# Kernel optimization log

Measured on AMD Instinct MI355X. Metric: run time of the kernel, lower is better.

The kernel has to match this reference:

```python
import jax, jax.numpy as jnp
import numpy as np

B, S, DM = 8, 1024, 1024
H, DH = 16, 64  # num_heads, per-head dim (q=k=v=r)
SCALE = 64 ** 1 / 2  # faithful to source: d_k**1/2 == d_k/2 == 32.0


def setup_inputs() -> dict:
    key = jax.random.key(0)
    ks = jax.random.split(key, 13)
    std = 1.0 / np.sqrt(DM)
    def lin(k):
        kw, kb = jax.random.split(k)
        W = jax.random.uniform(kw, (DM, H * DH), jnp.float32, -std, std)
        b = jax.random.uniform(kb, (H * DH,), jnp.float32, -std, std)
        return W, b
    Wq, bq = lin(ks[0]); Wk, bk = lin(ks[1]); Wv, bv = lin(ks[2]); Wr, br = lin(ks[3])
    Wo = jax.random.uniform(ks[4], (H * DH, DM), jnp.float32, -std, std)
    bo = jax.random.uniform(ks[5], (DM,), jnp.float32, -std, std)
    return {
        "value": jax.random.normal(ks[6], (B, S, DM), jnp.float32),
        "key": jax.random.normal(ks[7], (B, S, DM), jnp.float32),
        "query": jax.random.normal(ks[8], (B, S, DM), jnp.float32),
        "Wq": Wq, "bq": bq, "Wk": Wk, "bk": bk,
        "Wv": Wv, "bv": bv, "Wr": Wr, "br": br,
        "Wo": Wo, "bo": bo,
    }


def reference(value, key, query, Wq, bq, Wk, bk, Wv, bv, Wr, br, Wo, bo):
    b = query.shape[0]
    # projections -> [b, s, h, d] -> [b, h, s, d]
    q = (query @ Wq + bq).reshape(b, -1, H, DH).transpose(0, 2, 1, 3)
    k = (key @ Wk + bk).reshape(b, -1, H, DH).transpose(0, 2, 1, 3)
    v = (value @ Wv + bv).reshape(b, -1, H, DH).transpose(0, 2, 1, 3)
    r = (query @ Wr + br).reshape(b, -1, H, DH).transpose(0, 2, 1, 3)
    energy = jnp.einsum('bhid,bhjd->bhij', q, k)
    attn = jax.nn.softmax(energy / SCALE, axis=-1)
    ctx = jnp.einsum('bhjd,bhij->bhid', v, attn)
    gated = (ctx * r).transpose(0, 2, 1, 3)  # R-gating, back to [b, s, h, d]
    out = gated.reshape(b, -1, H * DH) @ Wo + bo
    return out
```

## Files before the change

kernel.cpp:

```cpp
#include <hip/hip_runtime.h>
#include <stdint.h>

#define B_ 8
#define S_ 1024
#define DM_ 1024
#define H_ 16
#define DH_ 64
#define M_ (B_*S_)

typedef unsigned short u16;
typedef unsigned int u32;
typedef __attribute__((ext_vector_type(8))) short bf16x8;
typedef __attribute__((ext_vector_type(4))) float f32x4;

__device__ __forceinline__ u16 f2bf(float f){
  union { float f; u32 u; } x; x.f = f;
  u32 r = x.u + 0x7fffu + ((x.u >> 16) & 1u);
  return (u16)(r >> 16);
}
__device__ __forceinline__ float bf2f(u16 u){
  union { u32 u; float f; } x; x.u = ((u32)u) << 16; return x.f;
}
__device__ __forceinline__ u32 cvtpk(float lo, float hi){
  u32 r; asm("v_cvt_pk_bf16_f32 %0, %1, %2" : "=v"(r) : "v"(lo), "v"(hi)); return r;
}
__device__ __forceinline__ void gload16(const void* g, void* l){
  __builtin_amdgcn_global_load_lds((const __attribute__((address_space(1))) void*)g,
                                   (__attribute__((address_space(3))) void*)l, 16, 0, 0);
}

__global__ void k_cvt_act(const float* __restrict__ v, const float* __restrict__ k,
                          const float* __restrict__ q, u16* __restrict__ vb,
                          u16* __restrict__ kb, u16* __restrict__ qb){
  int z = blockIdx.y;
  const float* src = (z == 0) ? v : (z == 1) ? k : q;
  u16* dst = (z == 0) ? vb : (z == 1) ? kb : qb;
  size_t i = ((size_t)blockIdx.x * blockDim.x + threadIdx.x) * 8;
  float4 a = *(const float4*)(src + i);
  float4 b = *(const float4*)(src + i + 4);
  uint4 o;
  o.x = (u32)f2bf(a.x) | ((u32)f2bf(a.y) << 16);
  o.y = (u32)f2bf(a.z) | ((u32)f2bf(a.w) << 16);
  o.z = (u32)f2bf(b.x) | ((u32)f2bf(b.y) << 16);
  o.w = (u32)f2bf(b.z) | ((u32)f2bf(b.w) << 16);
  *(uint4*)(dst + i) = o;
}

__global__ void k_cvt_wt(const float* __restrict__ w0, const float* __restrict__ w1,
                         const float* __restrict__ w2, const float* __restrict__ w3,
                         const float* __restrict__ w4,
                         u16* __restrict__ wall, u16* __restrict__ wot){
  __shared__ float tile[32][33];
  int z = blockIdx.z;
  const float* src = (z==0)?w0:(z==1)?w1:(z==2)?w2:(z==3)?w3:w4;
  u16* dst = (z<4) ? (wall + (size_t)z * 1048576) : wot;
  int n0 = blockIdx.x * 32, k0 = blockIdx.y * 32;
  int tx = threadIdx.x, ty = threadIdx.y;
#pragma unroll
  for (int i=0;i<4;i++) tile[ty+8*i][tx] = src[(size_t)(k0+ty+8*i)*DM_ + n0+tx];
  __syncthreads();
#pragma unroll
  for (int i=0;i<4;i++) dst[(size_t)(n0+ty+8*i)*DM_ + k0+tx] = f2bf(tile[tx][ty+8*i]);
}

__global__ __launch_bounds__(256) void k_proj(const u16* __restrict__ qb, const u16* __restrict__ kb,
                                              const u16* __restrict__ vb, const u16* __restrict__ wall,
                                              const float* __restrict__ bqp, const float* __restrict__ brp,
                                              const float* __restrict__ bkp, const float* __restrict__ bvp,
                                              u16* __restrict__ qpj, u16* __restrict__ rpj,
                                              u16* __restrict__ kpj, u16* __restrict__ vtg){
  __shared__ u16 As[128*64];
  __shared__ u16 Bs[128*64];
  const int tid = threadIdx.x;
  const int w = tid >> 6, l = tid & 63, g = l >> 4, s = l & 15;
  const int wr = w >> 1, wc = w & 1;
  const int m0 = blockIdx.x << 7;
  const int ng0 = blockIdx.y << 7;
  const int chunk = ng0 >> 10;
  const u16* A = (chunk < 2) ? qb : (chunk == 2) ? kb : vb;
  const float* bias = (chunk==0)?bqp:(chunk==1)?brp:(chunk==2)?bkp:bvp;
  f32x4 acc[4][4];
#pragma unroll
  for (int i=0;i<4;i++)
#pragma unroll
    for (int j=0;j<4;j++) acc[i][j] = (f32x4){0.f,0.f,0.f,0.f};

  for (int k0 = 0; k0 < 1024; k0 += 64){
    __syncthreads();
#pragma unroll
    for (int i=0;i<4;i++){
      int c = tid + i*256;
      int m = c >> 3, slot = c & 7;
      gload16(A + ((size_t)(m0+m) << 10) + (k0 + ((slot ^ (m & 7)) << 3)),
              &As[(i*256 + w*64) * 8]);
    }
#pragma unroll
    for (int i=0;i<4;i++){
      int c = tid + i*256;
      int n = c >> 3, slot = c & 7;
      gload16(wall + ((size_t)(ng0+n) << 10) + (k0 + ((slot ^ (n & 7)) << 3)),
              &Bs[(i*256 + w*64) * 8]);
    }
    __syncthreads();
#pragma unroll
    for (int ks=0; ks<2; ks++){
      bf16x8 af[4], bfv[4];
#pragma unroll
      for (int mi=0;mi<4;mi++){
        int m = wr*64 + mi*16 + s;
        af[mi] = *(const bf16x8*)&As[m*64 + (((ks*4+g) ^ (s & 7)) << 3)];
      }
#pragma unroll
      for (int ni=0;ni<4;ni++){
        int n = wc*64 + ni*16 + s;
        bfv[ni] = *(const bf16x8*)&Bs[n*64 + (((ks*4+g) ^ (s & 7)) << 3)];
      }
#pragma unroll
      for (int mi=0;mi<4;mi++)
#pragma unroll
        for (int ni=0;ni<4;ni++)
          acc[mi][ni] = __builtin_amdgcn_mfma_f32_16x16x32_bf16(af[mi], bfv[ni], acc[mi][ni], 0, 0, 0);
    }
  }
  u16* outp = (chunk==0)?qpj:(chunk==1)?rpj:kpj;
#pragma unroll
  for (int ni=0;ni<4;ni++){
    int cg = ng0 + wc*64 + ni*16 + s;
    int col = cg & 1023;
    float bv = bias[col];
#pragma unroll
    for (int mi=0;mi<4;mi++){
      int row = m0 + wr*64 + mi*16 + g*4;
      if (chunk == 3){
        union { short4 v; u16 e[4]; } pk;
#pragma unroll
        for (int r=0;r<4;r++) pk.e[r] = f2bf(acc[mi][ni][r] + bv);
        size_t vrow = ((size_t)(row >> 10) * 16 + (col >> 6)) * 64 + (col & 63);
        *(short4*)&vtg[(vrow << 10) + (row & 1023)] = pk.v;
      } else {
#pragma unroll
        for (int r=0;r<4;r++)
          outp[((size_t)(row+r) << 10) + col] = f2bf(acc[mi][ni][r] + bv);
      }
    }
  }
}

__global__ __launch_bounds__(256) void k_gemm_out(const u16* __restrict__ A, const u16* __restrict__ Bt,
                                                  const float* __restrict__ bias, float* __restrict__ Out){
  __shared__ u16 As[128*64];
  __shared__ u16 Bs[128*64];
  const int tid = threadIdx.x;
  const int w = tid >> 6, l = tid & 63, g = l >> 4, s = l & 15;
  const int wr = w >> 1, wc = w & 1;
  const int m0 = blockIdx.x << 7, n0 = blockIdx.y << 7;
  f32x4 acc[4][4];
#pragma unroll
  for (int i=0;i<4;i++)
#pragma unroll
    for (int j=0;j<4;j++) acc[i][j] = (f32x4){0.f,0.f,0.f,0.f};

  for (int k0 = 0; k0 < 1024; k0 += 64){
    __syncthreads();
#pragma unroll
    for (int i=0;i<4;i++){
      int c = tid + i*256;
      int m = c >> 3, slot = c & 7;
      gload16(A + ((size_t)(m0+m) << 10) + (k0 + ((slot ^ (m & 7)) << 3)),
              &As[(i*256 + w*64) * 8]);
    }
#pragma unroll
    for (int i=0;i<4;i++){
      int c = tid + i*256;
      int n = c >> 3, slot = c & 7;
      gload16(Bt + ((size_t)(n0+n) << 10) + (k0 + ((slot ^ (n & 7)) << 3)),
              &Bs[(i*256 + w*64) * 8]);
    }
    __syncthreads();
#pragma unroll
    for (int ks=0; ks<2; ks++){
      bf16x8 af[4], bfv[4];
#pragma unroll
      for (int mi=0;mi<4;mi++){
        int m = wr*64 + mi*16 + s;
        af[mi] = *(const bf16x8*)&As[m*64 + (((ks*4+g) ^ (s & 7)) << 3)];
      }
#pragma unroll
      for (int ni=0;ni<4;ni++){
        int n = wc*64 + ni*16 + s;
        bfv[ni] = *(const bf16x8*)&Bs[n*64 + (((ks*4+g) ^ (s & 7)) << 3)];
      }
#pragma unroll
      for (int mi=0;mi<4;mi++)
#pragma unroll
        for (int ni=0;ni<4;ni++)
          acc[mi][ni] = __builtin_amdgcn_mfma_f32_16x16x32_bf16(af[mi], bfv[ni], acc[mi][ni], 0, 0, 0);
    }
  }
#pragma unroll
  for (int ni=0;ni<4;ni++){
    int col = n0 + wc*64 + ni*16 + s;
    float bv = bias[col];
#pragma unroll
    for (int mi=0;mi<4;mi++){
      int row = m0 + wr*64 + mi*16 + g*4;
#pragma unroll
      for (int r=0;r<4;r++)
        Out[((size_t)(row+r) << 10) + col] = acc[mi][ni][r] + bv;
    }
  }
}

__global__ __launch_bounds__(256) void k_attn(const u16* __restrict__ qp, const u16* __restrict__ kp,
                                              const u16* __restrict__ vtg, const u16* __restrict__ rp,
                                              u16* __restrict__ gated){
  __shared__ u16 Ks[2][64*64];
  __shared__ u16 Vs[2][64*64];
  __shared__ u32 PsU[4*16*32];
  const int tid = threadIdx.x;
  const int w = tid >> 6, l = tid & 63, g = l >> 4, s = l & 15;
  const int bid = blockIdx.x;
  const int swz = (bid & 7) * 256 + (bid >> 3);
  const int q0 = (swz & 15) << 6;
  const int bh = swz >> 4;
  const int b = bh >> 4, h = bh & 15;
  const size_t base = ((size_t)b << 20);
  const int colh = h << 6;
  const float KL = 1.4426950408889634f / 32.0f;

  const size_t qoff = base + ((size_t)(q0 + w*16 + s) << 10) + colh;
  bf16x8 qf0 = *(const bf16x8*)(qp + qoff + g*8);
  bf16x8 qf1 = *(const bf16x8*)(qp + qoff + 32 + g*8);
  const size_t vbase = ((size_t)(b*16 + h)) << 16;

  u32* PsW = PsU + (w << 9);
  const int sx2 = s << 1;

  float mrun = -1e30f, lsum = 0.f;
  f32x4 of[4];
#pragma unroll
  for (int d=0;d<4;d++) of[d] = (f32x4){0.f,0.f,0.f,0.f};

#define STAGE_KV(BUF, KV0) do { \
    _Pragma("unroll") \
    for (int i=0;i<2;i++){ \
      int c = tid + i*256; \
      int sj = c >> 3, slot = c & 7; \
      gload16(kp + base + ((size_t)((KV0)+sj) << 10) + colh + ((slot ^ (sj & 7)) << 3), \
              &Ks[BUF][(i*256 + w*64) * 8]); \
    } \
    _Pragma("unroll") \
    for (int i=0;i<2;i++){ \
      int c = tid + i*256; \
      int d = c >> 3, slot = c & 7; \
      gload16(vtg + vbase + ((size_t)d << 10) + (KV0) + ((slot ^ (d & 7)) << 3), \
              &Vs[BUF][(i*256 + w*64) * 8]); \
    } \
  } while(0)

  STAGE_KV(0, 0);
  __syncthreads();

  int cur = 0;
  for (int t = 0; t < 16; t++){
    if (t < 15) STAGE_KV(cur ^ 1, (t+1) << 6);
    const u16* ksb = Ks[cur];
    const u16* vsb = Vs[cur];

    f32x4 e2[4];
#pragma unroll
    for (int sjf=0;sjf<4;sjf++){
      e2[sjf] = (f32x4){0.f,0.f,0.f,0.f};
      int sj = sjf*16 + s;
      bf16x8 kf0 = *(const bf16x8*)&ksb[sj*64 + ((g ^ (s & 7)) << 3)];
      e2[sjf] = __builtin_amdgcn_mfma_f32_16x16x32_bf16(kf0, qf0, e2[sjf], 0, 0, 0);
      bf16x8 kf1 = *(const bf16x8*)&ksb[sj*64 + (((4+g) ^ (s & 7)) << 3)];
      e2[sjf] = __builtin_amdgcn_mfma_f32_16x16x32_bf16(kf1, qf1, e2[sjf], 0, 0, 0);
    }
    float rm = fmaxf(fmaxf(e2[0][0], e2[0][1]), e2[0][2]);
    rm = fmaxf(fmaxf(rm, e2[0][3]), e2[1][0]);
    rm = fmaxf(fmaxf(rm, e2[1][1]), e2[1][2]);
    rm = fmaxf(fmaxf(rm, e2[1][3]), e2[2][0]);
    rm = fmaxf(fmaxf(rm, e2[2][1]), e2[2][2]);
    rm = fmaxf(fmaxf(rm, e2[2][3]), e2[3][0]);
    rm = fmaxf(fmaxf(rm, e2[3][1]), e2[3][2]);
    rm = fmaxf(rm, e2[3][3]);
    rm = fmaxf(rm, __shfl_xor(rm, 16, 64));
    rm = fmaxf(rm, __shfl_xor(rm, 32, 64));
    if (!__all(rm <= mrun + 177.0f)){
      float nm = fmaxf(mrun, rm);
      float alpha = __builtin_amdgcn_exp2f((mrun - nm) * KL);
      mrun = nm;
      lsum *= alpha;
      float ac[4];
#pragma unroll
      for (int r=0;r<4;r++) ac[r] = __shfl(alpha, g*4 + r, 64);
#pragma unroll
      for (int d=0; d<4; d++)
#pragma unroll
        for (int r=0;r<4;r++) of[d][r] *= ac[r];
    }

    const float mk = mrun * KL;
#pragma unroll
    for (int sjf=0;sjf<4;sjf++){
      float p0 = __builtin_amdgcn_exp2f(e2[sjf][0]*KL - mk);
      float p1 = __builtin_amdgcn_exp2f(e2[sjf][1]*KL - mk);
      float p2 = __builtin_amdgcn_exp2f(e2[sjf][2]*KL - mk);
      float p3 = __builtin_amdgcn_exp2f(e2[sjf][3]*KL - mk);
      lsum += (p0 + p1) + (p2 + p3);
      uint2 pk; pk.x = cvtpk(p0, p1); pk.y = cvtpk(p2, p3);
      int phys = (8*sjf + 2*g) ^ sx2;
      *reinterpret_cast<uint2*>(&PsW[(s << 5) + phys]) = pk;
    }
    union { u32 u[4]; bf16x8 v; } pa0, pa1;
    {
      uint2 r0 = *reinterpret_cast<const uint2*>(&PsW[(s << 5) + ((4*g    ) ^ sx2)]);
      uint2 r1 = *reinterpret_cast<const uint2*>(&PsW[(s << 5) + ((4*g + 2) ^ sx2)]);
      pa0.u[0] = r0.x; pa0.u[1] = r0.y; pa0.u[2] = r1.x; pa0.u[3] = r1.y;
      uint2 r2 = *reinterpret_cast<const uint2*>(&PsW[(s << 5) + ((16 + 4*g    ) ^ sx2)]);
      uint2 r3 = *reinterpret_cast<const uint2*>(&PsW[(s << 5) + ((16 + 4*g + 2) ^ sx2)]);
      pa1.u[0] = r2.x; pa1.u[1] = r2.y; pa1.u[2] = r3.x; pa1.u[3] = r3.y;
    }
#pragma unroll
    for (int df=0; df<4; df++){
      int d = df*16 + s;
      bf16x8 v0 = *(const bf16x8*)&vsb[d*64 + ((g ^ (s & 7)) << 3)];
      bf16x8 v1 = *(const bf16x8*)&vsb[d*64 + (((4+g) ^ (s & 7)) << 3)];
      of[df] = __builtin_amdgcn_mfma_f32_16x16x32_bf16(pa0.v, v0, of[df], 0, 0, 0);
      of[df] = __builtin_amdgcn_mfma_f32_16x16x32_bf16(pa1.v, v1, of[df], 0, 0, 0);
    }
    __syncthreads();
    cur ^= 1;
  }
#undef STAGE_KV

  lsum += __shfl_xor(lsum, 16, 64);
  lsum += __shfl_xor(lsum, 32, 64);
  float inv = 1.0f / lsum;
  float ic[4];
#pragma unroll
  for (int r=0;r<4;r++) ic[r] = __shfl(inv, g*4 + r, 64);
#pragma unroll
  for (int df=0; df<4; df++){
#pragma unroll
    for (int r=0;r<4;r++){
      size_t row = (size_t)(q0 + w*16 + g*4 + r);
      size_t idx = base + (row << 10) + colh + df*16 + s;
      float o = of[df][r] * ic[r];
      float rg = bf2f(rp[idx]);
      gated[idx] = f2bf(o * rg);
    }
  }
}

extern "C" void kernel_launch(void* const* d_in, const int* in_sizes, int n_in,
                              void* d_out, int out_size, void* d_ws, size_t ws_size,
                              hipStream_t stream){
  (void)in_sizes; (void)n_in; (void)out_size; (void)ws_size;
  const float* value = (const float*)d_in[0];
  const float* key   = (const float*)d_in[1];
  const float* query = (const float*)d_in[2];
  const float* Wq = (const float*)d_in[3];  const float* bq = (const float*)d_in[4];
  const float* Wk = (const float*)d_in[5];  const float* bk = (const float*)d_in[6];
  const float* Wv = (const float*)d_in[7];  const float* bv = (const float*)d_in[8];
  const float* Wr = (const float*)d_in[9];  const float* br = (const float*)d_in[10];
  const float* Wo = (const float*)d_in[11]; const float* bo = (const float*)d_in[12];

  char* ws = (char*)d_ws;
  const size_t MB = (size_t)1 << 20;
  u16* qb   = (u16*)(ws + 0*MB);
  u16* kb   = (u16*)(ws + 16*MB);
  u16* vb   = (u16*)(ws + 32*MB);
  u16* wall = (u16*)(ws + 48*MB);
  u16* wot  = (u16*)(ws + 56*MB);
  u16* qpj  = (u16*)(ws + 58*MB);
  u16* kpj  = (u16*)(ws + 74*MB);
  u16* vtg  = (u16*)(ws + 90*MB);
  u16* rpj  = (u16*)(ws + 106*MB);
  u16* gat  = qb;

  k_cvt_act<<<dim3(4096, 3), 256, 0, stream>>>(value, key, query, vb, kb, qb);
  k_cvt_wt<<<dim3(32, 32, 5), dim3(32, 8), 0, stream>>>(Wq, Wr, Wk, Wv, Wo, wall, wot);
  k_proj<<<dim3(64, 32), 256, 0, stream>>>(qb, kb, vb, wall, bq, br, bk, bv,
                                           qpj, rpj, kpj, vtg);
  k_attn<<<2048, 256, 0, stream>>>(qpj, kpj, vtg, rpj, gat);
  k_gemm_out<<<dim3(64, 8), 256, 0, stream>>>(gat, wot, bo, (float*)d_out);
}
```

Before: 210.2 us.

## Rewrite projection GEMM as 256x256 tile, 8-wave double-buffered pipelined kernel

Replaces the 128x128, 4-wave projection GEMM with a 256x256 tile kernel using 8 waves and 128 KB of dynamic LDS. A and B tiles are double-buffered, and global loads for the next k-tiles are interleaved with MFMA phases using explicit barriers, vmcnt waits and s_setprio. The aim is to hide global load latency behind compute and to raise arithmetic intensity through larger tiles. In exchange it uses more LDS and registers, which lowers occupancy. The launch grid shrinks to 512 blocks, so there is a risk of tail imbalance.

```diff
diff --git a/kernel.cpp b/kernel.cpp
--- a/kernel.cpp
+++ b/kernel.cpp
@@ -63,80 +63,133 @@
   for (int i=0;i<4;i++) dst[(size_t)(n0+ty+8*i)*DM_ + k0+tx] = f2bf(tile[tx][ty+8*i]);
 }
 
-__global__ __launch_bounds__(256) void k_proj(const u16* __restrict__ qb, const u16* __restrict__ kb,
-                                              const u16* __restrict__ vb, const u16* __restrict__ wall,
-                                              const float* __restrict__ bqp, const float* __restrict__ brp,
-                                              const float* __restrict__ bkp, const float* __restrict__ bvp,
-                                              u16* __restrict__ qpj, u16* __restrict__ rpj,
-                                              u16* __restrict__ kpj, u16* __restrict__ vtg){
-  __shared__ u16 As[128*64];
-  __shared__ u16 Bs[128*64];
+__global__ __launch_bounds__(512, 2) void k_proj8(const u16* __restrict__ qb, const u16* __restrict__ kb,
+                                                  const u16* __restrict__ vb, const u16* __restrict__ wall,
+                                                  const float* __restrict__ bqp, const float* __restrict__ brp,
+                                                  const float* __restrict__ bkp, const float* __restrict__ bvp,
+                                                  u16* __restrict__ qpj, u16* __restrict__ rpj,
+                                                  u16* __restrict__ kpj, u16* __restrict__ vtg){
+  extern __shared__ u16 smem[];
+  u16* As = smem;
+  u16* Bs = smem + 32768;
   const int tid = threadIdx.x;
   const int w = tid >> 6, l = tid & 63, g = l >> 4, s = l & 15;
-  const int wr = w >> 1, wc = w & 1;
-  const int m0 = blockIdx.x << 7;
-  const int ng0 = blockIdx.y << 7;
+  const int wr = w >> 2, wc = w & 3;
+  const int m0 = blockIdx.x << 8;
+  const int ng0 = blockIdx.y << 8;
   const int chunk = ng0 >> 10;
   const u16* A = (chunk < 2) ? qb : (chunk == 2) ? kb : vb;
+
+  f32x4 acc[8][4];
+#pragma unroll
+  for (int i=0;i<8;i++)
+#pragma unroll
+    for (int j=0;j<4;j++) acc[i][j] = (f32x4){0.f,0.f,0.f,0.f};
+
+#define PSTAGE_A(buf, tile, h) do { \
+    int k0s = (tile) << 6; \
+    _Pragma("unroll") \
+    for (int i2 = 0; i2 < 2; i2++){ \
+      int c = tid + i2*512; int rw = c >> 3, sl = c & 7; \
+      gload16(A + ((size_t)(m0 + (h)*128 + rw) << 10) + k0s + ((sl ^ (rw & 7)) << 3), \
+              &As[(buf)*16384 + (h)*8192 + (i2*512 + w*64)*8]); \
+    } } while(0)
+
+#define PSTAGE_B(buf, tile, h) do { \
+    int k0s = (tile) << 6; \
+    _Pragma("unroll") \
+    for (int i2 = 0; i2 < 2; i2++){ \
+      int c = tid + i2*512; int rw = c >> 3, sl = c & 7; \
+      gload16(wall + ((size_t)(ng0 + (h)*128 + rw) << 10) + k0s + ((sl ^ (rw & 7)) << 3), \
+              &Bs[(buf)*16384 + (h)*8192 + (i2*512 + w*64)*8]); \
+    } } while(0)
+
+#define PLOADA(cb, mh) do { \
+    _Pragma("unroll") for (int mi2=0; mi2<4; mi2++) \
+    _Pragma("unroll") for (int ks=0; ks<2; ks++){ \
+      int rw = wr*128 + (mh)*64 + mi2*16 + s; \
+      af[mi2][ks] = *(const bf16x8*)&As[(cb)*16384 + rw*64 + (((ks*4+g) ^ (s&7)) << 3)]; \
+    } } while(0)
+
+#define PLOADB(dst, cb, nh) do { \
+    _Pragma("unroll") for (int ni2=0; ni2<2; ni2++) \
+    _Pragma("unroll") for (int ks=0; ks<2; ks++){ \
+      int rw = wc*64 + (nh)*32 + ni2*16 + s; \
+      dst[ni2][ks] = *(const bf16x8*)&Bs[(cb)*16384 + rw*64 + (((ks*4+g) ^ (s&7)) << 3)]; \
+    } } while(0)
+
+#define PMFMA(mh, nh, bfr) do { \
+    _Pragma("unroll") for (int mi2=0; mi2<4; mi2++) \
+    _Pragma("unroll") for (int ni2=0; ni2<2; ni2++) \
+    _Pragma("unroll") for (int ks=0; ks<2; ks++) \
+      acc[(mh)*4+mi2][(nh)*2+ni2] = __builtin_amdgcn_mfma_f32_16x16x32_bf16( \
+          af[mi2][ks], bfr[ni2][ks], acc[(mh)*4+mi2][(nh)*2+ni2], 0, 0, 0); \
+    } while(0)
+
+#define BAR   __builtin_amdgcn_s_barrier()
+#define PRIO1 __builtin_amdgcn_s_setprio(1)
+#define PRIO0 __builtin_amdgcn_s_setprio(0)
+
+  PSTAGE_A(0, 0, 0); PSTAGE_A(0, 0, 1); PSTAGE_B(0, 0, 0); PSTAGE_B(0, 0, 1);
+  PSTAGE_B(1, 1, 0); PSTAGE_B(1, 1, 1);
+  asm volatile("s_waitcnt vmcnt(4)" ::: "memory");
+  BAR;
+
+#pragma unroll 1
+  for (int it = 0; it < 8; ++it){
+    const int tB = 2*it + 1, t2 = 2*it + 2, t3 = 2*it + 3;
+    const bool pre = (it < 7);
+    {
+      bf16x8 af[4][2], bf0[2][2], bf1[2][2];
+      PLOADA(0, 0); PLOADB(bf0, 0, 0);
+      PSTAGE_A(1, tB, 0);
+      BAR; PRIO1; PMFMA(0, 0, bf0); PRIO0; BAR;
+      PLOADB(bf1, 0, 1);
+      PSTAGE_A(1, tB, 1);
+      BAR; PRIO1; PMFMA(0, 1, bf1); PRIO0; BAR;
+      PLOADA(0, 1);
+      if (pre) PSTAGE_B(0, t2, 0);
+      BAR; PRIO1; PMFMA(1, 1, bf1); PRIO0; BAR;
+      if (pre) PSTAGE_B(0, t2, 1);
+      BAR; PRIO1; PMFMA(1, 0, bf0); PRIO0;
+      if (it == 7) asm volatile("s_waitcnt vmcnt(0)" ::: "memory");
+      else         asm volatile("s_waitcnt vmcnt(4)" ::: "memory");
+      BAR;
+    }
+    {
+      bf16x8 af[4][2], bf0[2][2], bf1[2][2];
+      PLOADA(1, 0); PLOADB(bf0, 1, 0);
+      if (pre) PSTAGE_A(0, t2, 0);
+      BAR; PRIO1; PMFMA(0, 0, bf0); PRIO0; BAR;
+      PLOADB(bf1, 1, 1);
+      if (pre) PSTAGE_A(0, t2, 1);
+      BAR; PRIO1; PMFMA(0, 1, bf1); PRIO0; BAR;
+      PLOADA(1, 1);
+      if (pre) PSTAGE_B(1, t3, 0);
+      BAR; PRIO1; PMFMA(1, 1, bf1); PRIO0; BAR;
+      if (pre) PSTAGE_B(1, t3, 1);
+      BAR; PRIO1; PMFMA(1, 0, bf0); PRIO0;
+      asm volatile("s_waitcnt vmcnt(4)" ::: "memory");
+      BAR;
+    }
+  }
+
   const float* bias = (chunk==0)?bqp:(chunk==1)?brp:(chunk==2)?bkp:bvp;
-  f32x4 acc[4][4];
-#pragma unroll
-  for (int i=0;i<4;i++)
-#pragma unroll
-    for (int j=0;j<4;j++) acc[i][j] = (f32x4){0.f,0.f,0.f,0.f};
-
-  for (int k0 = 0; k0 < 1024; k0 += 64){
-    __syncthreads();
-#pragma unroll
-    for (int i=0;i<4;i++){
-      int c = tid + i*256;
-      int m = c >> 3, slot = c & 7;
-      gload16(A + ((size_t)(m0+m) << 10) + (k0 + ((slot ^ (m & 7)) << 3)),
-              &As[(i*256 + w*64) * 8]);
-    }
-#pragma unroll
-    for (int i=0;i<4;i++){
-      int c = tid + i*256;
-      int n = c >> 3, slot = c & 7;
-      gload16(wall + ((size_t)(ng0+n) << 10) + (k0 + ((slot ^ (n & 7)) << 3)),
-              &Bs[(i*256 + w*64) * 8]);
-    }
-    __syncthreads();
-#pragma unroll
-    for (int ks=0; ks<2; ks++){
-      bf16x8 af[4], bfv[4];
-#pragma unroll
-      for (int mi=0;mi<4;mi++){
-        int m = wr*64 + mi*16 + s;
-        af[mi] = *(const bf16x8*)&As[m*64 + (((ks*4+g) ^ (s & 7)) << 3)];
-      }
-#pragma unroll
-      for (int ni=0;ni<4;ni++){
-        int n = wc*64 + ni*16 + s;
-        bfv[ni] = *(const bf16x8*)&Bs[n*64 + (((ks*4+g) ^ (s & 7)) << 3)];
-      }
-#pragma unroll
-      for (int mi=0;mi<4;mi++)
-#pragma unroll
-        for (int ni=0;ni<4;ni++)
-          acc[mi][ni] = __builtin_amdgcn_mfma_f32_16x16x32_bf16(af[mi], bfv[ni], acc[mi][ni], 0, 0, 0);
-    }
-  }
   u16* outp = (chunk==0)?qpj:(chunk==1)?rpj:kpj;
 #pragma unroll
-  for (int ni=0;ni<4;ni++){
+  for (int ni=0; ni<4; ni++){
     int cg = ng0 + wc*64 + ni*16 + s;
     int col = cg & 1023;
     float bv = bias[col];
 #pragma unroll
-    for (int mi=0;mi<4;mi++){
-      int row = m0 + wr*64 + mi*16 + g*4;
+    for (int mi=0; mi<8; mi++){
+      int row = m0 + wr*128 + mi*16 + g*4;
       if (chunk == 3){
-        union { short4 v; u16 e[4]; } pk;
-#pragma unroll
-        for (int r=0;r<4;r++) pk.e[r] = f2bf(acc[mi][ni][r] + bv);
+        union { short4 v; u16 e[4]; } pk2;
+#pragma unroll
+        for (int r=0;r<4;r++) pk2.e[r] = f2bf(acc[mi][ni][r] + bv);
         size_t vrow = ((size_t)(row >> 10) * 16 + (col >> 6)) * 64 + (col & 63);
-        *(short4*)&vtg[(vrow << 10) + (row & 1023)] = pk.v;
+        *(short4*)&vtg[(vrow << 10) + (row & 1023)] = pk2.v;
       } else {
 #pragma unroll
         for (int r=0;r<4;r++)
@@ -144,6 +197,14 @@
       }
     }
   }
+#undef PSTAGE_A
+#undef PSTAGE_B
+#undef PLOADA
+#undef PLOADB
+#undef PMFMA
+#undef BAR
+#undef PRIO1
+#undef PRIO0
 }
 
 __global__ __launch_bounds__(256) void k_gemm_out(const u16* __restrict__ A, const u16* __restrict__ Bt,
@@ -380,10 +441,13 @@
   u16* rpj  = (u16*)(ws + 106*MB);
   u16* gat  = qb;
 
+  (void)hipFuncSetAttribute(reinterpret_cast<const void*>(&k_proj8),
+                            hipFuncAttributeMaxDynamicSharedMemorySize, 131072);
+
   k_cvt_act<<<dim3(4096, 3), 256, 0, stream>>>(value, key, query, vb, kb, qb);
   k_cvt_wt<<<dim3(32, 32, 5), dim3(32, 8), 0, stream>>>(Wq, Wr, Wk, Wv, Wo, wall, wot);
-  k_proj<<<dim3(64, 32), 256, 0, stream>>>(qb, kb, vb, wall, bq, br, bk, bv,
-                                           qpj, rpj, kpj, vtg);
+  k_proj8<<<dim3(32, 16), 512, 131072, stream>>>(qb, kb, vb, wall, bq, br, bk, bv,
+                                                 qpj, rpj, kpj, vtg);
   k_attn<<<2048, 256, 0, stream>>>(qpj, kpj, vtg, rpj, gat);
   k_gemm_out<<<dim3(64, 8), 256, 0, stream>>>(gat, wot, bo, (float*)d_out);
 }
```

Result: faster. 197.7 us (-5.9%).
